# Kernel tuning notes

Measured on AMD Instinct MI355X. Metric: run time of the kernel, lower is better.

Reference implementation:

```python
import jax, jax.numpy as jnp
import numpy as np

HO, WO = 64, 64
SHARPNESS = 150.0


def _stereographic_grid(ho, wo):
    # Matches create_normal_grid(..., 'stereographic'); torch.meshgrid 'ij':
    # v varies over rows (ho), u over cols (wo).
    v, u = np.meshgrid(np.arange(ho), np.arange(wo), indexing='ij')
    p = 4.0 * ((u + 0.5) / wo - 0.5)
    q = -4.0 * ((v + 0.5) / ho - 0.5)
    d = 1.0 + p ** 2 + q ** 2
    z = -(-1.0 + p ** 2 + q ** 2) / d
    m = (z > 0.0).astype(np.float32)
    x = 2.0 * p / d * m
    y = 2.0 * q / d * m
    z = z * m
    return np.stack([x, y, z], axis=-1).reshape(-1, 3).astype(np.float32)  # [ho*wo,3]


_GRID = _stereographic_grid(HO, WO)
_IDX = np.nonzero(np.any(_GRID != 0, axis=-1))[0]  # static valid-query indices [N]
_QN = _GRID[_IDX]  # [N,3]


def setup_inputs() -> dict:
    key = jax.random.key(0)
    k1, k2, k3 = jax.random.split(key, 3)
    bs, c, h, w = 2, 64, 192, 192
    in_fea_map = jax.random.normal(k1, (bs, c, h, w), dtype=jnp.float32)
    nrm = jax.random.normal(k2, (bs, 3, h, w), dtype=jnp.float32)
    in_normal_map = nrm / (jnp.linalg.norm(nrm, axis=1, keepdims=True) + 1e-8)
    in_mask_map = (jax.random.uniform(k3, (bs, 1, h, w)) > 0.2).astype(jnp.float32)
    log_query_norm = jnp.full((1,), np.log(SHARPNESS), dtype=jnp.float32)
    return {"in_fea_map": in_fea_map, "in_normal_map": in_normal_map,
            "in_mask_map": in_mask_map, "log_query_norm": log_query_norm}


def reference(in_fea_map, in_normal_map, in_mask_map, log_query_norm):
    bs, c, h, w = in_fea_map.shape
    hw = h * w
    qn = jnp.asarray(_QN, dtype=in_fea_map.dtype)  # [N,3] static valid queries
    vals = in_fea_map.reshape(bs, c, hw).transpose(0, 2, 1)       # [bs,HW,c]
    key_n = in_normal_map.reshape(bs, 3, hw)                       # [bs,3,HW]
    cos = jnp.einsum('nd,bdm->bnm', qn, key_n)                     # [bs,N,HW]
    dps = cos / np.float32(np.sqrt(3.0))
    dps = dps - jnp.max(dps, axis=-1, keepdims=True)
    w_ = jnp.exp(jnp.exp(log_query_norm) * dps)                    # dropout in eval = identity
    w_ = w_ * in_mask_map.reshape(bs, 1, hw)
    weights = w_ / (jnp.sum(w_, axis=-1, keepdims=True) + 1e-9)    # [bs,N,HW]
    mapped = weights @ vals                                        # [bs,N,c]
    mapped = jnp.concatenate([jnp.broadcast_to(qn, (bs,) + qn.shape), mapped], axis=-1)
    # variance map over last 3 feature channels
    mean = mapped[..., -3:]
    sq_mean = weights @ (vals[..., -3:] ** 2)
    var = jnp.sum(sq_mean - mean ** 2, axis=-1, keepdims=True)
    mapped = jnp.concatenate([var, mapped], axis=-1)
    # cosine map
    rm_cos = jnp.sum(weights * cos, axis=-1, keepdims=True)
    mapped = jnp.concatenate([rm_cos, mapped], axis=-1)            # [bs,N,c+5]
    C = mapped.shape[-1]
    out = jnp.zeros((bs, HO * WO, C), mapped.dtype).at[:, _IDX, :].set(mapped)
    return out.transpose(0, 2, 1).reshape(bs, C, HO, WO)
```

## Files before the change

### kernel.cpp

```cpp
#include <hip/hip_runtime.h>
#include <hip/hip_bf16.h>
#include <cstdint>
#include <cstddef>

#define HW 36864
#define QT 128
#define NCHA 69

constexpr bool is_valid_px(int v, int u) {
  int a = 2 * u - 63, b = 2 * v - 63;
  return a * a + b * b < 1024;
}
constexpr int count_valid() {
  int n = 0;
  for (int v = 0; v < 64; ++v)
    for (int u = 0; u < 64; ++u)
      if (is_valid_px(v, u)) ++n;
  return n;
}
constexpr int NV  = count_valid();
constexpr int NQT = (NV + QT - 1) / QT;
constexpr int NQP = NQT * QT;
constexpr int PLANE = 2 * NQP * NCHA;

struct QTab {
  short idx[NQP];
  short rank[4096];
};
constexpr QTab make_qtab() {
  QTab t{};
  int n = 0;
  for (int p = 0; p < 4096; ++p) {
    int v = p >> 6, u = p & 63;
    if (is_valid_px(v, u)) { t.idx[n] = (short)p; t.rank[p] = (short)n; ++n; }
    else t.rank[p] = -1;
  }
  for (int i = n; i < NQP; ++i) t.idx[i] = -1;
  return t;
}
__constant__ QTab g_qtab = make_qtab();

typedef short short8 __attribute__((ext_vector_type(8)));
typedef float f32x4  __attribute__((ext_vector_type(4)));

__device__ __forceinline__ ushort2 f2b2(float a, float b) {
  __hip_bfloat162 h = __float22bfloat162_rn(make_float2(a, b));
  return *(ushort2*)&h;
}
__device__ __forceinline__ short8 cvt8(float4 a, float4 b) {
  short8 o;
  ushort2 p0 = f2b2(a.x, a.y), p1 = f2b2(a.z, a.w);
  ushort2 p2 = f2b2(b.x, b.y), p3 = f2b2(b.z, b.w);
  o[0] = (short)p0.x; o[1] = (short)p0.y; o[2] = (short)p1.x; o[3] = (short)p1.y;
  o[4] = (short)p2.x; o[5] = (short)p2.y; o[6] = (short)p3.x; o[7] = (short)p3.y;
  return o;
}
__device__ __forceinline__ void pix2qn(int pix, float& x, float& y, float& z) {
  x = 0.f; y = 0.f; z = 0.f;
  if (pix >= 0) {
    int v = pix >> 6, u = pix & 63;
    float p = (float)(2 * u - 63) * (1.0f / 32.0f);
    float q = -(float)(2 * v - 63) * (1.0f / 32.0f);
    float d = 1.0f + p * p + q * q;
    x = 2.0f * p / d; y = 2.0f * q / d; z = (1.0f - p * p - q * q) / d;
  }
}

template<int KSC>
__global__ __launch_bounds__(256, 4) void partial_kernel(
    const float* __restrict__ fea,
    const float* __restrict__ nrm,
    const float* __restrict__ msk,
    const float* __restrict__ lqn,
    float* __restrict__ part)
{
  constexpr int SLICE  = HW / KSC;
  constexpr int NCHUNK = SLICE / 64;

  __shared__ __align__(16) unsigned short v_s[2][80][72];
  __shared__ __align__(16) float nrm4_s[2][64][4];

  const int bx  = blockIdx.x;
  const int cls = bx & 7;
  const int r0  = bx >> 3;
  const int qt  = r0 % NQT;
  const int sh  = r0 / NQT;
  const int s   = sh * 8 + cls;
  const int b   = s / KSC;
  const int ks  = s % KSC;

  const int t    = threadIdx.x;
  const int wv   = t >> 6;
  const int l    = t & 63;
  const int lq   = l >> 4;
  const int mrow = l & 15;

  const float Cc = __expf(lqn[0]) * 0.57735026919f;

  float qx[2], qy[2], qz[2];
  pix2qn(g_qtab.idx[qt * QT + 32 * wv + mrow],      qx[0], qy[0], qz[0]);
  pix2qn(g_qtab.idx[qt * QT + 32 * wv + 16 + mrow], qx[1], qy[1], qz[1]);

  const int c0 = (t & 7) * 8;
  const int rg = t >> 3;
  const int pxp = 32 * (l >> 5) + 4 * (l & 7) + ((l >> 3) & 3);

  f32x4 acc[2][5];
  #pragma unroll
  for (int h = 0; h < 2; ++h)
    #pragma unroll
    for (int nt = 0; nt < 5; ++nt) acc[h][nt] = (f32x4)(0.0f);

  float4 pF[6];
  float nx, ny, nz, mk;
  const size_t feab = (size_t)b * 64 * HW;
  const size_t nrmb = (size_t)b * 3 * HW;
  const size_t mskb = (size_t)b * HW;
  const int ckb = ks * NCHUNK;

  if (t >= 48 && t < 128) {
    int row = 64 + rg;
    short cv = (row == 70) ? (short)0x3F80 : (short)0;
    short8 o;
    #pragma unroll
    for (int i = 0; i < 8; ++i) o[i] = cv;
    *(short8*)&v_s[0][row][c0] = o;
    *(short8*)&v_s[1][row][c0] = o;
  }

  auto load_chunk = [&](int ck) {
    const size_t p0 = (size_t)((ckb + ck) * 64);
    if (t < 64) {
      size_t px = p0 + (size_t)l;
      nx = nrm[nrmb + px];
      ny = nrm[nrmb + HW + px];
      nz = nrm[nrmb + 2 * HW + px];
      mk = msk[mskb + px];
    }
    const float* fb = fea + feab + p0 + c0;
    pF[0] = *(const float4*)(fb + (size_t)rg * HW);
    pF[1] = *(const float4*)(fb + (size_t)rg * HW + 4);
    pF[2] = *(const float4*)(fb + (size_t)(rg + 32) * HW);
    pF[3] = *(const float4*)(fb + (size_t)(rg + 32) * HW + 4);
    if (t < 48) {
      const float* srcb = (t < 24)
          ? (fea + feab + (size_t)(61 + rg) * HW)
          : (nrm + nrmb + (size_t)(rg - 3) * HW);
      pF[4] = *(const float4*)(srcb + p0 + c0);
      pF[5] = *(const float4*)(srcb + p0 + c0 + 4);
    }
  };
  auto store_chunk = [&](int buf) {
    if (t < 64)
      *(float4*)&nrm4_s[buf][pxp][0] =
          make_float4(Cc * nx, Cc * ny, Cc * nz,
                      -Cc + (mk > 0.5f ? 0.f : -2000.f));
    *(short8*)&v_s[buf][rg][c0]      = cvt8(pF[0], pF[1]);
    *(short8*)&v_s[buf][rg + 32][c0] = cvt8(pF[2], pF[3]);
    if (t < 48) {
      float4 a = pF[4], bq = pF[5];
      if (t < 24) {
        a.x *= a.x; a.y *= a.y; a.z *= a.z; a.w *= a.w;
        bq.x *= bq.x; bq.y *= bq.y; bq.z *= bq.z; bq.w *= bq.w;
      }
      *(short8*)&v_s[buf][64 + rg][c0] = cvt8(a, bq);
    }
  };

  load_chunk(0);
  store_chunk(0);
  __syncthreads();

  for (int ck = 0; ck < NCHUNK; ++ck) {
    const int buf = ck & 1;
    if (ck + 1 < NCHUNK) load_chunk(ck + 1);

    #pragma unroll
    for (int kh = 0; kh < 2; ++kh) {
      float e0[8], e1[8];
      #pragma unroll
      for (int j = 0; j < 8; ++j) {
        const float4 nvv = *(const float4*)&nrm4_s[buf][32 * kh + 4 * j + lq][0];
        float t0 = fmaf(qx[0], nvv.x, fmaf(qy[0], nvv.y, fmaf(qz[0], nvv.z, nvv.w)));
        float t1 = fmaf(qx[1], nvv.x, fmaf(qy[1], nvv.y, fmaf(qz[1], nvv.z, nvv.w)));
        e0[j] = __expf(t0);
        e1[j] = __expf(t1);
      }
      short8 a0, a1;
      #pragma unroll
      for (int p = 0; p < 4; ++p) {
        ushort2 p0 = f2b2(e0[2 * p], e0[2 * p + 1]);
        ushort2 p1 = f2b2(e1[2 * p], e1[2 * p + 1]);
        a0[2 * p] = (short)p0.x; a0[2 * p + 1] = (short)p0.y;
        a1[2 * p] = (short)p1.x; a1[2 * p + 1] = (short)p1.y;
      }
      #pragma unroll
      for (int nt = 0; nt < 5; ++nt) {
        short8 bb = *(const short8*)&v_s[buf][16 * nt + mrow][32 * kh + 8 * lq];
        acc[0][nt] = __builtin_amdgcn_mfma_f32_16x16x32_bf16(a0, bb, acc[0][nt], 0, 0, 0);
        acc[1][nt] = __builtin_amdgcn_mfma_f32_16x16x32_bf16(a1, bb, acc[1][nt], 0, 0, 0);
      }
    }

    if (ck + 1 < NCHUNK) {
      store_chunk(buf ^ 1);
      __syncthreads();
    }
  }

  __syncthreads();
  float* exs = (float*)&v_s[0][0][0];

  const size_t pbase = (size_t)ks * PLANE + ((size_t)b * NQP + (size_t)(qt * QT)) * NCHA;
  #pragma unroll
  for (int h = 0; h < 2; ++h) {
    #pragma unroll
    for (int nt = 0; nt < 4; ++nt)
      #pragma unroll
      for (int rr = 0; rr < 4; ++rr) {
        int qloc = 32 * wv + 16 * h + 4 * lq + rr;
        part[pbase + (size_t)qloc * NCHA + (size_t)(16 * nt + mrow)] = acc[h][nt][rr];
      }
    if (mrow < 7) {
      #pragma unroll
      for (int rr = 0; rr < 4; ++rr)
        exs[(32 * wv + 16 * h + 4 * lq + rr) * 9 + mrow] = acc[h][4][rr];
    }
  }
  __syncthreads();
  if (t < QT) {
    float gx, gy, gz;
    pix2qn(g_qtab.idx[qt * QT + t], gx, gy, gz);
    const float* E = exs + t * 9;
    float swc = gx * E[3] + gy * E[4] + gz * E[5];
    size_t o = pbase + (size_t)t * NCHA;
    part[o + 64] = E[0];
    part[o + 65] = E[1];
    part[o + 66] = E[2];
    part[o + 67] = swc;
    part[o + 68] = E[6];
  }
}

#define NFIN 448
#define NTAIL (2 * NFIN)

__global__ __launch_bounds__(256) void finalize_kernel(
    const float* __restrict__ part,
    float* __restrict__ out,
    int ksc)
{
  const int blk = blockIdx.x;
  const int t   = threadIdx.x;

  if (blk < NFIN) {
    __shared__ float sm[4][NCHA];
    const int b   = blk / (NFIN / 2);
    const int rem = blk % (NFIN / 2);
    const int q0  = rem * 4;

    const size_t colbase = ((size_t)b * NQP + (size_t)q0) * NCHA;
    for (int i = t; i < 4 * NCHA; i += 256) {
      float sv = 0.f;
      const size_t off = colbase + (size_t)i;
      #pragma unroll 8
      for (int k = 0; k < ksc; ++k) sv += part[(size_t)k * PLANE + off];
      sm[0][i] = sv;
    }
    __syncthreads();

    for (int i = t; i < 4 * NCHA; i += 256) {
      const int ql = i / NCHA;
      const int oc = i % NCHA;
      const int pix = g_qtab.idx[q0 + ql];
      if (pix < 0) continue;
      const float* A = sm[ql];
      const float inv = 1.0f / (A[68] + 1e-9f);
      float gx, gy, gz;
      pix2qn(pix, gx, gy, gz);
      float val;
      if (oc == 0)      val = A[67] * inv;
      else if (oc == 1) {
        val = 0.f;
        #pragma unroll
        for (int j = 0; j < 3; ++j) {
          float m  = A[61 + j] * inv;
          float sq = A[64 + j] * inv;
          val += sq - m * m;
        }
      }
      else if (oc == 2) val = gx;
      else if (oc == 3) val = gy;
      else if (oc == 4) val = gz;
      else              val = A[oc - 5] * inv;
      out[((size_t)b * NCHA + (size_t)oc) * 4096 + pix] = val;
    }
  } else {
    const int start = (blk - NFIN) * 256 + t;
    const int strd  = (NTAIL - NFIN) * 256;
    const int TOT   = 2 * NCHA * 4096;
    for (int i = start; i < TOT; i += strd) {
      if (g_qtab.rank[i & 4095] < 0) out[i] = 0.0f;
    }
  }
}

extern "C" void kernel_launch(void* const* d_in, const int* in_sizes, int n_in,
                              void* d_out, int out_size, void* d_ws, size_t ws_size,
                              hipStream_t stream) {
  const float* fea = (const float*)d_in[0];
  const float* nrm = (const float*)d_in[1];
  const float* msk = (const float*)d_in[2];
  const float* lqn = (const float*)d_in[3];
  float* part = (float*)d_ws;
  float* out  = (float*)d_out;

  const size_t need64 = (size_t)64 * PLANE * sizeof(float);
  const size_t need32 = (size_t)32 * PLANE * sizeof(float);
  if (ws_size >= need64) {
    partial_kernel<64><<<dim3(2 * 64 * NQT), 256, 0, stream>>>(fea, nrm, msk, lqn, part);
    finalize_kernel<<<dim3(NTAIL), 256, 0, stream>>>(part, out, 64);
  } else if (ws_size >= need32) {
    partial_kernel<32><<<dim3(2 * 32 * NQT), 256, 0, stream>>>(fea, nrm, msk, lqn, part);
    finalize_kernel<<<dim3(NTAIL), 256, 0, stream>>>(part, out, 32);
  } else {
    partial_kernel<16><<<dim3(2 * 16 * NQT), 256, 0, stream>>>(fea, nrm, msk, lqn, part);
    finalize_kernel<<<dim3(NTAIL), 256, 0, stream>>>(part, out, 16);
  }
}
```

Before: 107.9 us.

## Halve partial-kernel block to 128 threads with four query tiles per wave

Each partial_kernel block now runs 2 waves instead of 4, and each wave handles 64 queries (four 16-row MFMA tiles) instead of 32. Each B-fragment read from LDS therefore feeds four MFMAs, and each normal read feeds four exps. Every thread now loads four feature rows per chunk instead of two, and the padding-row init and epilogue indexing are adjusted to match. The cost is many more accumulator and prefetch registers, lower launch-bound occupancy (2 blocks of 2 waves), and less latency hiding for global loads.

```diff
diff --git a/kernel.cpp b/kernel.cpp
--- a/kernel.cpp
+++ b/kernel.cpp
@@ -67,7 +67,7 @@
 }
 
 template<int KSC>
-__global__ __launch_bounds__(256, 4) void partial_kernel(
+__global__ __launch_bounds__(128, 2) void partial_kernel(
     const float* __restrict__ fea,
     const float* __restrict__ nrm,
     const float* __restrict__ msk,
@@ -97,35 +97,38 @@
 
   const float Cc = __expf(lqn[0]) * 0.57735026919f;
 
-  float qx[2], qy[2], qz[2];
-  pix2qn(g_qtab.idx[qt * QT + 32 * wv + mrow],      qx[0], qy[0], qz[0]);
-  pix2qn(g_qtab.idx[qt * QT + 32 * wv + 16 + mrow], qx[1], qy[1], qz[1]);
+  float qx[4], qy[4], qz[4];
+  #pragma unroll
+  for (int h = 0; h < 4; ++h)
+    pix2qn(g_qtab.idx[qt * QT + 64 * wv + 16 * h + mrow], qx[h], qy[h], qz[h]);
 
   const int c0 = (t & 7) * 8;
   const int rg = t >> 3;
   const int pxp = 32 * (l >> 5) + 4 * (l & 7) + ((l >> 3) & 3);
 
-  f32x4 acc[2][5];
+  f32x4 acc[4][5];
   #pragma unroll
-  for (int h = 0; h < 2; ++h)
+  for (int h = 0; h < 4; ++h)
     #pragma unroll
     for (int nt = 0; nt < 5; ++nt) acc[h][nt] = (f32x4)(0.0f);
 
-  float4 pF[6];
+  float4 pF[10];
   float nx, ny, nz, mk;
   const size_t feab = (size_t)b * 64 * HW;
   const size_t nrmb = (size_t)b * 3 * HW;
   const size_t mskb = (size_t)b * HW;
   const int ckb = ks * NCHUNK;
 
-  if (t >= 48 && t < 128) {
-    int row = 64 + rg;
+  if (t >= 48) {
+    int idx = t - 48;
+    int row = 70 + (idx >> 3);
+    int col = (idx & 7) * 8;
     short cv = (row == 70) ? (short)0x3F80 : (short)0;
     short8 o;
     #pragma unroll
     for (int i = 0; i < 8; ++i) o[i] = cv;
-    *(short8*)&v_s[0][row][c0] = o;
-    *(short8*)&v_s[1][row][c0] = o;
+    *(short8*)&v_s[0][row][col] = o;
+    *(short8*)&v_s[1][row][col] = o;
   }
 
   auto load_chunk = [&](int ck) {
@@ -138,16 +141,17 @@
       mk = msk[mskb + px];
     }
     const float* fb = fea + feab + p0 + c0;
-    pF[0] = *(const float4*)(fb + (size_t)rg * HW);
-    pF[1] = *(const float4*)(fb + (size_t)rg * HW + 4);
-    pF[2] = *(const float4*)(fb + (size_t)(rg + 32) * HW);
-    pF[3] = *(const float4*)(fb + (size_t)(rg + 32) * HW + 4);
+    #pragma unroll
+    for (int i = 0; i < 4; ++i) {
+      pF[2 * i]     = *(const float4*)(fb + (size_t)(rg + 16 * i) * HW);
+      pF[2 * i + 1] = *(const float4*)(fb + (size_t)(rg + 16 * i) * HW + 4);
+    }
     if (t < 48) {
       const float* srcb = (t < 24)
           ? (fea + feab + (size_t)(61 + rg) * HW)
           : (nrm + nrmb + (size_t)(rg - 3) * HW);
-      pF[4] = *(const float4*)(srcb + p0 + c0);
-      pF[5] = *(const float4*)(srcb + p0 + c0 + 4);
+      pF[8] = *(const float4*)(srcb + p0 + c0);
+      pF[9] = *(const float4*)(srcb + p0 + c0 + 4);
     }
   };
   auto store_chunk = [&](int buf) {
@@ -155,10 +159,11 @@
       *(float4*)&nrm4_s[buf][pxp][0] =
           make_float4(Cc * nx, Cc * ny, Cc * nz,
                       -Cc + (mk > 0.5f ? 0.f : -2000.f));
-    *(short8*)&v_s[buf][rg][c0]      = cvt8(pF[0], pF[1]);
-    *(short8*)&v_s[buf][rg + 32][c0] = cvt8(pF[2], pF[3]);
+    #pragma unroll
+    for (int i = 0; i < 4; ++i)
+      *(short8*)&v_s[buf][rg + 16 * i][c0] = cvt8(pF[2 * i], pF[2 * i + 1]);
     if (t < 48) {
-      float4 a = pF[4], bq = pF[5];
+      float4 a = pF[8], bq = pF[9];
       if (t < 24) {
         a.x *= a.x; a.y *= a.y; a.z *= a.z; a.w *= a.w;
         bq.x *= bq.x; bq.y *= bq.y; bq.z *= bq.z; bq.w *= bq.w;
@@ -177,28 +182,38 @@
 
     #pragma unroll
     for (int kh = 0; kh < 2; ++kh) {
-      float e0[8], e1[8];
+      float e0[8], e1[8], e2[8], e3[8];
       #pragma unroll
       for (int j = 0; j < 8; ++j) {
         const float4 nvv = *(const float4*)&nrm4_s[buf][32 * kh + 4 * j + lq][0];
         float t0 = fmaf(qx[0], nvv.x, fmaf(qy[0], nvv.y, fmaf(qz[0], nvv.z, nvv.w)));
         float t1 = fmaf(qx[1], nvv.x, fmaf(qy[1], nvv.y, fmaf(qz[1], nvv.z, nvv.w)));
+        float t2 = fmaf(qx[2], nvv.x, fmaf(qy[2], nvv.y, fmaf(qz[2], nvv.z, nvv.w)));
+        float t3 = fmaf(qx[3], nvv.x, fmaf(qy[3], nvv.y, fmaf(qz[3], nvv.z, nvv.w)));
         e0[j] = __expf(t0);
         e1[j] = __expf(t1);
-      }
-      short8 a0, a1;
+        e2[j] = __expf(t2);
+        e3[j] = __expf(t3);
+      }
+      short8 a0, a1, a2, a3;
       #pragma unroll
       for (int p = 0; p < 4; ++p) {
         ushort2 p0 = f2b2(e0[2 * p], e0[2 * p + 1]);
         ushort2 p1 = f2b2(e1[2 * p], e1[2 * p + 1]);
+        ushort2 p2 = f2b2(e2[2 * p], e2[2 * p + 1]);
+        ushort2 p3 = f2b2(e3[2 * p], e3[2 * p + 1]);
         a0[2 * p] = (short)p0.x; a0[2 * p + 1] = (short)p0.y;
         a1[2 * p] = (short)p1.x; a1[2 * p + 1] = (short)p1.y;
+        a2[2 * p] = (short)p2.x; a2[2 * p + 1] = (short)p2.y;
+        a3[2 * p] = (short)p3.x; a3[2 * p + 1] = (short)p3.y;
       }
       #pragma unroll
       for (int nt = 0; nt < 5; ++nt) {
         short8 bb = *(const short8*)&v_s[buf][16 * nt + mrow][32 * kh + 8 * lq];
         acc[0][nt] = __builtin_amdgcn_mfma_f32_16x16x32_bf16(a0, bb, acc[0][nt], 0, 0, 0);
         acc[1][nt] = __builtin_amdgcn_mfma_f32_16x16x32_bf16(a1, bb, acc[1][nt], 0, 0, 0);
+        acc[2][nt] = __builtin_amdgcn_mfma_f32_16x16x32_bf16(a2, bb, acc[2][nt], 0, 0, 0);
+        acc[3][nt] = __builtin_amdgcn_mfma_f32_16x16x32_bf16(a3, bb, acc[3][nt], 0, 0, 0);
       }
     }
 
@@ -213,22 +228,22 @@
 
   const size_t pbase = (size_t)ks * PLANE + ((size_t)b * NQP + (size_t)(qt * QT)) * NCHA;
   #pragma unroll
-  for (int h = 0; h < 2; ++h) {
+  for (int h = 0; h < 4; ++h) {
     #pragma unroll
     for (int nt = 0; nt < 4; ++nt)
       #pragma unroll
       for (int rr = 0; rr < 4; ++rr) {
-        int qloc = 32 * wv + 16 * h + 4 * lq + rr;
+        int qloc = 64 * wv + 16 * h + 4 * lq + rr;
         part[pbase + (size_t)qloc * NCHA + (size_t)(16 * nt + mrow)] = acc[h][nt][rr];
       }
     if (mrow < 7) {
       #pragma unroll
       for (int rr = 0; rr < 4; ++rr)
-        exs[(32 * wv + 16 * h + 4 * lq + rr) * 9 + mrow] = acc[h][4][rr];
+        exs[(64 * wv + 16 * h + 4 * lq + rr) * 9 + mrow] = acc[h][4][rr];
     }
   }
   __syncthreads();
-  if (t < QT) {
+  {
     float gx, gy, gz;
     pix2qn(g_qtab.idx[qt * QT + t], gx, gy, gz);
     const float* E = exs + t * 9;
@@ -318,13 +333,13 @@
   const size_t need64 = (size_t)64 * PLANE * sizeof(float);
   const size_t need32 = (size_t)32 * PLANE * sizeof(float);
   if (ws_size >= need64) {
-    partial_kernel<64><<<dim3(2 * 64 * NQT), 256, 0, stream>>>(fea, nrm, msk, lqn, part);
+    partial_kernel<64><<<dim3(2 * 64 * NQT), 128, 0, stream>>>(fea, nrm, msk, lqn, part);
     finalize_kernel<<<dim3(NTAIL), 256, 0, stream>>>(part, out, 64);
   } else if (ws_size >= need32) {
-    partial_kernel<32><<<dim3(2 * 32 * NQT), 256, 0, stream>>>(fea, nrm, msk, lqn, part);
+    partial_kernel<32><<<dim3(2 * 32 * NQT), 128, 0, stream>>>(fea, nrm, msk, lqn, part);
     finalize_kernel<<<dim3(NTAIL), 256, 0, stream>>>(part, out, 32);
   } else {
-    partial_kernel<16><<<dim3(2 * 16 * NQT), 256, 0, stream>>>(fea, nrm, msk, lqn, part);
+    partial_kernel<16><<<dim3(2 * 16 * NQT), 128, 0, stream>>>(fea, nrm, msk, lqn, part);
     finalize_kernel<<<dim3(NTAIL), 256, 0, stream>>>(part, out, 16);
   }
 }
```

Result: slower. 110.8 us (+2.7%).
